# Optimization experiments

Measured on AMD Instinct MI355X. Metric: run time of the kernel, lower is better.

## Reference

```python
import jax, jax.numpy as jnp
import numpy as np

NUM_HEADS = 8


def setup_inputs() -> dict:
    key = jax.random.key(0)
    ks = jax.random.split(key, 7)
    B, D, N = 16, 512, 2048
    sc = 1.0 / np.sqrt(D)
    return {
        "X_Query": jax.random.normal(ks[0], (B, D, N), jnp.float32),
        "X_Key": jax.random.normal(ks[1], (B, D, N), jnp.float32),
        "X_Value": jax.random.normal(ks[2], (B, D, N), jnp.float32),
        "W_q": jax.random.normal(ks[3], (D, D), jnp.float32) * sc,
        "W_k": jax.random.normal(ks[4], (D, D), jnp.float32) * sc,
        "W_v": jax.random.normal(ks[5], (D, D), jnp.float32) * sc,
        "W_o": jax.random.normal(ks[6], (D, D), jnp.float32) * sc,
    }


def _proj(W, x):
    # Conv1d(D, D, kernel_size=1, bias=False) == channel matmul
    return jnp.einsum('oi,bin->bon', W, x)


def _split_heads(x, h):
    # torch: cat(x.chunk(h, dim=-1), dim=0) -> (h, B, D, N/h) stacked layout
    B, D, N = x.shape
    return x.reshape(B, D, h, N // h).transpose(2, 0, 1, 3)


def _mha(XQ, XK, XV, Wq, Wk, Wv, Wo):
    B, D, N = XQ.shape
    h = NUM_HEADS
    Nh = N // h
    q = _split_heads(_proj(Wq, XQ), h)  # (h, B, D, Nh)
    k = _split_heads(_proj(Wk, XK), h)
    v = _split_heads(_proj(Wv, XV), h)
    # scores over the CHANNEL axis: (h, B, D, D), scaled by sqrt(d_k)=sqrt(Nh)
    scores = jnp.einsum('hbdn,hben->hbde', q, k) / jnp.sqrt(jnp.asarray(Nh, q.dtype))
    p = jax.nn.softmax(scores, axis=-1)
    out = jnp.einsum('hbde,hben->hbdn', p, v)  # (h, B, D, Nh)
    # torch: cat(chunks, dim=0) inverse -> cat along dim=-1
    attn_heads = out.transpose(1, 2, 0, 3).reshape(B, D, N)
    return _proj(Wo, XQ - attn_heads)


def reference(X_Query, X_Key, X_Value, W_q, W_k, W_v, W_o):
    return _mha(X_Query, X_Key, X_Value, W_q, W_k, W_v, W_o)
```

## Files before the change

kernel.cpp:

```cpp
#include <hip/hip_runtime.h>
#include <hip/hip_bf16.h>

#define DD  512
#define NN  2048
#define BB  16
#define NHD 256

typedef unsigned short u16;
typedef __attribute__((ext_vector_type(4))) float f32x4;
typedef __attribute__((ext_vector_type(8))) short s16x8;
typedef __attribute__((ext_vector_type(4))) u16   u16x4;

static __device__ __forceinline__ u16 f2bf(float f) {
  __hip_bfloat16 h = __float2bfloat16(f);
  return *reinterpret_cast<u16*>(&h);
}
static __device__ __forceinline__ float bf2f(u16 u) {
  union { unsigned int i; float f; } v; v.i = ((unsigned int)u) << 16; return v.f;
}
static __device__ __forceinline__ f32x4 mfma_bf16(s16x8 a, s16x8 b, f32x4 c) {
  return __builtin_amdgcn_mfma_f32_16x16x32_bf16(a, b, c, 0, 0, 0);
}
static __device__ __forceinline__ void gload_lds16(const u16* g, u16* l) {
  __builtin_amdgcn_global_load_lds(
      (const __attribute__((address_space(1))) unsigned int*)g,
      (__attribute__((address_space(3))) unsigned int*)l, 16, 0, 0);
}
static __device__ __forceinline__ void barrier_raw() {
  __builtin_amdgcn_sched_barrier(0);
  __builtin_amdgcn_s_barrier();
  __builtin_amdgcn_sched_barrier(0);
}
#define WAITCNT(s) do { asm volatile("s_waitcnt " s ::: "memory"); \
                        __builtin_amdgcn_sched_barrier(0); } while (0)

__global__ __launch_bounds__(256) void k_cvt_w(const float* __restrict__ w0,
                                               const float* __restrict__ w1,
                                               const float* __restrict__ w2,
                                               const float* __restrict__ w3,
                                               u16* __restrict__ out) {
  const float* srcs[4] = {w0, w1, w2, w3};
  const float* s = srcs[blockIdx.y];
  u16* o = out + (size_t)blockIdx.y * (DD * DD);
  int idx = blockIdx.x * 256 + threadIdx.x;
  float4 v = *(const float4*)(s + (size_t)idx * 4);
  u16x4 u = {f2bf(v.x), f2bf(v.y), f2bf(v.z), f2bf(v.w)};
  *(u16x4*)(o + (size_t)idx * 4) = u;
}

__global__ __launch_bounds__(256) void k_transpose(const float* __restrict__ X,
                                                   u16* __restrict__ XT) {
  __shared__ float t[64][68];
  const int tid = threadIdx.x;
  const int n0 = blockIdx.x * 64, d0 = blockIdx.y * 64, b = blockIdx.z;
  const float* Xb = X + ((size_t)b * DD + d0) * NN + n0;
#pragma unroll
  for (int i = 0; i < 4; ++i) {
    int r = (tid >> 4) + i * 16;
    int c = (tid & 15) * 4;
    float4 v = *(const float4*)(Xb + (size_t)r * NN + c);
    t[r][c] = v.x; t[r][c + 1] = v.y; t[r][c + 2] = v.z; t[r][c + 3] = v.w;
  }
  __syncthreads();
  u16* Ob = XT + ((size_t)b * NN + n0) * DD + d0;
#pragma unroll
  for (int i = 0; i < 4; ++i) {
    int n = (tid >> 4) + i * 16;
    int d = (tid & 15) * 4;
    u16x4 u = {f2bf(t[d][n]), f2bf(t[d + 1][n]), f2bf(t[d + 2][n]), f2bf(t[d + 3][n])};
    *(u16x4*)(Ob + (size_t)n * DD + d) = u;
  }
}

#define GEMM_STAGE(Ag, lda, Bg, ldb, buf, kt)                                   \
  {                                                                             \
    _Pragma("unroll")                                                           \
    for (int j = 0; j < 4; ++j) {                                               \
      int s = j * 256 + w * 64 + lane;                                          \
      int row = s >> 3, u = s & 7;                                              \
      int col = ((u ^ (row & 7)) * 8);                                          \
      gload_lds16(Ag + (size_t)row * lda + (kt) * 64 + col, &Ab[buf][s * 8]);   \
      gload_lds16(Bg + (size_t)row * ldb + (kt) * 64 + col, &Bb[buf][s * 8]);   \
    }                                                                           \
  }

#define GEMM_COMPUTE(buf)                                                       \
  {                                                                             \
    _Pragma("unroll")                                                           \
    for (int ks = 0; ks < 2; ++ks) {                                            \
      s16x8 av[4], bv[4];                                                       \
      _Pragma("unroll")                                                         \
      for (int m = 0; m < 4; ++m) {                                             \
        int row = wm + m * 16 + r;                                              \
        av[m] = *(const s16x8*)&Ab[buf][row * 64 + (((ks * 4 + g) ^ (row & 7)) * 8)]; \
      }                                                                         \
      _Pragma("unroll")                                                         \
      for (int nf = 0; nf < 4; ++nf) {                                          \
        int row = wn + nf * 16 + r;                                             \
        bv[nf] = *(const s16x8*)&Bb[buf][row * 64 + (((ks * 4 + g) ^ (row & 7)) * 8)]; \
      }                                                                         \
      _Pragma("unroll")                                                         \
      for (int m = 0; m < 4; ++m)                                               \
        _Pragma("unroll")                                                       \
        for (int nf = 0; nf < 4; ++nf)                                          \
          acc[m][nf] = mfma_bf16(av[m], bv[nf], acc[m][nf]);                    \
    }                                                                           \
  }

#define GEMM_PREAMBLE                                                           \
  __shared__ __align__(16) u16 Ab[2][128 * 64];                                 \
  __shared__ __align__(16) u16 Bb[2][128 * 64];                                 \
  const int tid = threadIdx.x;                                                  \
  const int lane = tid & 63, w = tid >> 6;                                      \
  const int wm = (w >> 1) * 64, wn = (w & 1) * 64;                              \
  const int r = lane & 15, g = lane >> 4;                                       \
  f32x4 acc[4][4] = {};

#define GEMM_MAINLOOP(Ag, lda, Bg, ldb, nkt)                                    \
  GEMM_STAGE(Ag, lda, Bg, ldb, 0, 0);                                           \
  __syncthreads();                                                              \
  for (int kt = 0; kt < (nkt) - 1; ++kt) {                                      \
    GEMM_STAGE(Ag, lda, Bg, ldb, (kt & 1) ^ 1, kt + 1);                         \
    GEMM_COMPUTE(kt & 1);                                                       \
    __syncthreads();                                                            \
  }                                                                             \
  GEMM_COMPUTE(((nkt) - 1) & 1);

template <typename OUT_T>
__global__ __launch_bounds__(256) void k_gemm_nt(
    const u16* __restrict__ A, long long a_bs, int lda,
    const u16* __restrict__ B, long long b_bs, int ldb,
    OUT_T* __restrict__ C, long long c_bs, int ldc, int K) {
  GEMM_PREAMBLE
  const int m0 = blockIdx.x * 128, n0 = blockIdx.y * 128;
  const u16* Ag = A + (size_t)blockIdx.z * a_bs + (size_t)m0 * lda;
  const u16* Bg = B + (size_t)blockIdx.z * b_bs + (size_t)n0 * ldb;
  const int nkt = K >> 6;
  GEMM_MAINLOOP(Ag, lda, Bg, ldb, nkt);

  OUT_T* Cg = C + (size_t)blockIdx.z * c_bs;
#pragma unroll
  for (int m = 0; m < 4; ++m)
#pragma unroll
    for (int nf = 0; nf < 4; ++nf)
#pragma unroll
      for (int j = 0; j < 4; ++j) {
        int row = m0 + wm + m * 16 + g * 4 + j;
        int col = n0 + wn + nf * 16 + r;
        float v = acc[m][nf][j];
        if constexpr (sizeof(OUT_T) == 2) Cg[(size_t)row * ldc + col] = f2bf(v);
        else                              Cg[(size_t)row * ldc + col] = v;
      }
}

__global__ __launch_bounds__(512, 4) void k_attn_fused(
    const u16* __restrict__ Qdn, const u16* __restrict__ Kdn,
    const u16* __restrict__ VT,  const u16* __restrict__ XqT,
    u16* __restrict__ And) {
  __shared__ __align__(16) u16 L[26624];
  u16* Kr = L;
  u16* Vr = L + 12288;
  char* Psb = (char*)(L + 24576);

  const int tid = threadIdx.x;
  const int lane = tid & 63, w = tid >> 6;
  const int r = lane & 15, g = lane >> 4;
  const int dq = w >> 1, eh = w & 1;
  const int nq = w >> 1, dh = w & 1;
  const int bid = blockIdx.x;
  const int dt = bid >> 7, hb = bid & 127;
  const int h = hb & 7, b = hb >> 3;
  const int d0 = dt * 64, hn0 = h * NHD;

  const u16* Qg = Qdn + ((size_t)b * DD + d0) * NN + hn0;
  const u16* Kg = Kdn + ((size_t)b * DD) * NN + hn0;
  const u16* Vg = VT + ((size_t)b * NN + hn0) * DD;

  auto stage_k = [&](int s) {
    const int e0 = (s >> 1) * 32, n0 = (s & 1) * 128;
    u16* dst = Kr + (s % 3) * 4096;
    int row = tid >> 4, u = tid & 15;
    gload_lds16(Kg + (size_t)(e0 + row) * NN + n0 + ((u ^ (row & 7)) * 8), dst + tid * 8);
  };
  auto stage_v = [&](int t) {
    const int e0 = (t >> 1) * 32, j = t & 1;
    u16* dst = Vr + (t % 3) * 4096;
    int rl = tid >> 2, u = tid & 3;
    int gn = (rl >> 5) * 64 + j * 32 + (rl & 31);
    gload_lds16(Vg + (size_t)gn * DD + e0 + ((u ^ (rl & 3)) * 8), dst + tid * 8);
  };

#pragma unroll
  for (int jj = 0; jj < 4; ++jj) {
    int s = jj * 512 + tid;
    int row = s >> 5, u = s & 31;
    gload_lds16(Qg + (size_t)row * NN + ((u ^ (row & 7)) * 8), L + s * 8);
  }
  WAITCNT("vmcnt(0)");
  barrier_raw();
  s16x8 qf[8];
  {
    const int qrow = dq * 16 + r;
#pragma unroll
    for (int k2 = 0; k2 < 8; ++k2)
      qf[k2] = *(const s16x8*)&L[qrow * 256 + (((k2 * 4 + g) ^ (qrow & 7)) * 8)];
  }
  WAITCNT("lgkmcnt(0)");
  barrier_raw();
  stage_k(0); stage_v(0); stage_k(1);

  float psum[4] = {};
  f32x4 acc_o[2][2][2] = {};

  for (int et = 0; et < 16; ++et) {
    f32x4 acc_s = {};
#pragma unroll
    for (int cn = 0; cn < 2; ++cn) {
      const int s = et * 2 + cn;
      if (cn == 0)      WAITCNT("vmcnt(2)");
      else if (et < 15) WAITCNT("vmcnt(2)");
      else              WAITCNT("vmcnt(1)");
      barrier_raw();
      if (s + 1 < 32) stage_v(s + 1);
      if (s + 2 < 32) stage_k(s + 2);
      const u16* kb = Kr + (s % 3) * 4096;
      const int rowe = eh * 16 + r;
      __builtin_amdgcn_s_setprio(1);
#pragma unroll
      for (int kq = 0; kq < 4; ++kq) {
        s16x8 bv = *(const s16x8*)&kb[rowe * 128 + (((kq * 4 + g) ^ (rowe & 7)) * 8)];
        acc_s = mfma_bf16(qf[cn * 4 + kq], bv, acc_s);
      }
      __builtin_amdgcn_s_setprio(0);
      WAITCNT("lgkmcnt(0)");
    }
#pragma unroll
    for (int j = 0; j < 4; ++j) {
      int rowd = dq * 16 + g * 4 + j;
      int cole = eh * 16 + r;
      float p = __expf(acc_s[j] * 0.0625f);
      psum[j] += p;
      *(u16*)(Psb + rowd * 64 + (((cole * 2) ^ ((rowd & 3) << 4)))) = f2bf(p);
    }
    WAITCNT("lgkmcnt(0)");
    if (et < 15) WAITCNT("vmcnt(3)");
    else         WAITCNT("vmcnt(0)");
    barrier_raw();
#pragma unroll
    for (int j = 0; j < 2; ++j) {
      const u16* vb = Vr + ((et * 2 + j) % 3) * 4096;
      s16x8 pb[2];
#pragma unroll
      for (int nf = 0; nf < 2; ++nf) {
        int rowd = dh * 32 + nf * 16 + r;
        pb[nf] = *(const s16x8*)(Psb + rowd * 64 + ((g * 16) ^ ((rowd & 3) << 4)));
      }
      __builtin_amdgcn_s_setprio(1);
#pragma unroll
      for (int ms = 0; ms < 2; ++ms) {
        int rl = nq * 32 + ms * 16 + r;
        s16x8 av = *(const s16x8*)((const char*)vb + rl * 64 + ((g * 16) ^ ((rl & 3) << 4)));
        acc_o[j][ms][0] = mfma_bf16(av, pb[0], acc_o[j][ms][0]);
        acc_o[j][ms][1] = mfma_bf16(av, pb[1], acc_o[j][ms][1]);
      }
      __builtin_amdgcn_s_setprio(0);
    }
    WAITCNT("lgkmcnt(0)");
    barrier_raw();
  }

  float* rs = (float*)L;
#pragma unroll
  for (int j = 0; j < 4; ++j) {
    float v = psum[j];
    v += __shfl_xor(v, 1);
    v += __shfl_xor(v, 2);
    v += __shfl_xor(v, 4);
    v += __shfl_xor(v, 8);
    if (r == 0) rs[w * 16 + g * 4 + j] = v;
  }
  __syncthreads();
  if (tid < 64) {
    int dqi = tid >> 4, i = tid & 15;
    rs[128 + tid] = 1.0f / (rs[(dqi * 2) * 16 + i] + rs[(dqi * 2 + 1) * 16 + i]);
  }
  __syncthreads();

  const u16* Xg = XqT + ((size_t)b * NN + hn0) * DD + d0;
  u16* Ag = And + ((size_t)b * NN + hn0) * DD + d0;
#pragma unroll
  for (int j = 0; j < 2; ++j)
#pragma unroll
    for (int ms = 0; ms < 2; ++ms)
#pragma unroll
      for (int nf = 0; nf < 2; ++nf) {
        const int dc = dh * 32 + nf * 16 + r;
        const float inv = rs[128 + dc];
#pragma unroll
        for (int jj = 0; jj < 4; ++jj) {
          const int npos = nq * 64 + j * 32 + ms * 16 + g * 4 + jj;
          float o = acc_o[j][ms][nf][jj] * inv;
          float xq = bf2f(Xg[(size_t)npos * DD + dc]);
          Ag[(size_t)npos * DD + dc] = f2bf(xq - o);
        }
      }
}

extern "C" void kernel_launch(void* const* d_in, const int* in_sizes, int n_in,
                              void* d_out, int out_size, void* d_ws, size_t ws_size,
                              hipStream_t stream) {
  const float* Xq = (const float*)d_in[0];
  const float* Xk = (const float*)d_in[1];
  const float* Xv = (const float*)d_in[2];
  const float* Wq = (const float*)d_in[3];
  const float* Wk = (const float*)d_in[4];
  const float* Wv = (const float*)d_in[5];
  const float* Wo = (const float*)d_in[6];
  float* out = (float*)d_out;

  char* ws = (char*)d_ws;
  const size_t MB = 1024 * 1024;
  u16* Wb  = (u16*)ws;
  u16* XqT = (u16*)(ws + 2 * MB);
  u16* Z2  = (u16*)(ws + 34 * MB);
  u16* And = Z2;
  u16* Qdn = (u16*)(ws + 66 * MB);
  u16* VTb = (u16*)d_out;
  u16* Kdn = (u16*)d_out + (size_t)BB * NN * DD;

  k_cvt_w<<<dim3(256, 4), 256, 0, stream>>>(Wq, Wk, Wv, Wo, Wb);

  k_transpose<<<dim3(NN / 64, DD / 64, BB), 256, 0, stream>>>(Xv, Z2);
  k_gemm_nt<u16><<<dim3(NN / 128, DD / 128, BB), 256, 0, stream>>>(
      Z2, (long long)NN * DD, DD,
      Wb + 2 * DD * DD, 0, DD,
      VTb, (long long)NN * DD, DD, DD);

  k_transpose<<<dim3(NN / 64, DD / 64, BB), 256, 0, stream>>>(Xq, XqT);
  k_gemm_nt<u16><<<dim3(DD / 128, NN / 128, BB), 256, 0, stream>>>(
      Wb, 0, DD,
      XqT, (long long)NN * DD, DD,
      Qdn, (long long)DD * NN, NN, DD);

  k_transpose<<<dim3(NN / 64, DD / 64, BB), 256, 0, stream>>>(Xk, Z2);
  k_gemm_nt<u16><<<dim3(DD / 128, NN / 128, BB), 256, 0, stream>>>(
      Wb + 1 * DD * DD, 0, DD,
      Z2, (long long)NN * DD, DD,
      Kdn, (long long)DD * NN, NN, DD);

  k_attn_fused<<<dim3(1024), 512, 0, stream>>>(Qdn, Kdn, VTb, XqT, And);

  k_gemm_nt<float><<<dim3(DD / 128, NN / 128, BB), 256, 0, stream>>>(
      Wb + 3 * DD * DD, 0, DD,
      And, (long long)NN * DD, DD,
      out, (long long)DD * NN, NN, DD);
}
```

Baseline: 251.2 us.

## Merge three transposes into one launch and pad P tile instead of swizzling

The three separate fp32-to-bf16 transpose launches for Xq, Xk and Xv become one kernel launch with a 3x z-grid, which needs a separate workspace buffer for XkT. Independently, the P tile in shared memory inside the attention kernel switches from an XOR-swizzled 64-byte row layout to a padded row stride of 36 elements, read as two 8-byte loads. The first cuts launch overhead and tail effects. The second changes the LDS bank-conflict pattern and the number of load instructions, and may be neutral or worse for the P reads.

```diff
diff --git a/kernel.cpp b/kernel.cpp
--- a/kernel.cpp
+++ b/kernel.cpp
@@ -9,6 +9,7 @@
 typedef unsigned short u16;
 typedef __attribute__((ext_vector_type(4))) float f32x4;
 typedef __attribute__((ext_vector_type(8))) short s16x8;
+typedef __attribute__((ext_vector_type(4))) short s16x4;
 typedef __attribute__((ext_vector_type(4))) u16   u16x4;
 
 static __device__ __forceinline__ u16 f2bf(float f) {
@@ -48,11 +49,18 @@
   *(u16x4*)(o + (size_t)idx * 4) = u;
 }
 
-__global__ __launch_bounds__(256) void k_transpose(const float* __restrict__ X,
-                                                   u16* __restrict__ XT) {
+__global__ __launch_bounds__(256) void k_transpose3(const float* __restrict__ x0,
+                                                    const float* __restrict__ x1,
+                                                    const float* __restrict__ x2,
+                                                    u16* __restrict__ o0,
+                                                    u16* __restrict__ o1,
+                                                    u16* __restrict__ o2) {
   __shared__ float t[64][68];
   const int tid = threadIdx.x;
-  const int n0 = blockIdx.x * 64, d0 = blockIdx.y * 64, b = blockIdx.z;
+  const int z = blockIdx.z, which = z >> 4, b = z & 15;
+  const float* X = which == 0 ? x0 : (which == 1 ? x1 : x2);
+  u16*       XT = which == 0 ? o0 : (which == 1 ? o1 : o2);
+  const int n0 = blockIdx.x * 64, d0 = blockIdx.y * 64;
   const float* Xb = X + ((size_t)b * DD + d0) * NN + n0;
 #pragma unroll
   for (int i = 0; i < 4; ++i) {
@@ -157,10 +165,10 @@
     const u16* __restrict__ Qdn, const u16* __restrict__ Kdn,
     const u16* __restrict__ VT,  const u16* __restrict__ XqT,
     u16* __restrict__ And) {
-  __shared__ __align__(16) u16 L[26624];
+  __shared__ __align__(16) u16 L[26880];
   u16* Kr = L;
   u16* Vr = L + 12288;
-  char* Psb = (char*)(L + 24576);
+  u16* Ps = L + 24576;
 
   const int tid = threadIdx.x;
   const int lane = tid & 63, w = tid >> 6;
@@ -240,7 +248,7 @@
       int cole = eh * 16 + r;
       float p = __expf(acc_s[j] * 0.0625f);
       psum[j] += p;
-      *(u16*)(Psb + rowd * 64 + (((cole * 2) ^ ((rowd & 3) << 4)))) = f2bf(p);
+      Ps[rowd * 36 + cole] = f2bf(p);
     }
     WAITCNT("lgkmcnt(0)");
     if (et < 15) WAITCNT("vmcnt(3)");
@@ -253,7 +261,9 @@
 #pragma unroll
       for (int nf = 0; nf < 2; ++nf) {
         int rowd = dh * 32 + nf * 16 + r;
-        pb[nf] = *(const s16x8*)(Psb + rowd * 64 + ((g * 16) ^ ((rowd & 3) << 4)));
+        s16x4 plo = *(const s16x4*)&Ps[rowd * 36 + g * 8];
+        s16x4 phi = *(const s16x4*)&Ps[rowd * 36 + g * 8 + 4];
+        pb[nf] = __builtin_shufflevector(plo, phi, 0, 1, 2, 3, 4, 5, 6, 7);
       }
       __builtin_amdgcn_s_setprio(1);
 #pragma unroll
@@ -322,30 +332,29 @@
   const size_t MB = 1024 * 1024;
   u16* Wb  = (u16*)ws;
   u16* XqT = (u16*)(ws + 2 * MB);
-  u16* Z2  = (u16*)(ws + 34 * MB);
-  u16* And = Z2;
+  u16* XvT = (u16*)(ws + 34 * MB);
+  u16* And = XvT;
   u16* Qdn = (u16*)(ws + 66 * MB);
+  u16* XkT = (u16*)(ws + 98 * MB);
   u16* VTb = (u16*)d_out;
   u16* Kdn = (u16*)d_out + (size_t)BB * NN * DD;
 
   k_cvt_w<<<dim3(256, 4), 256, 0, stream>>>(Wq, Wk, Wv, Wo, Wb);
 
-  k_transpose<<<dim3(NN / 64, DD / 64, BB), 256, 0, stream>>>(Xv, Z2);
+  k_transpose3<<<dim3(NN / 64, DD / 64, BB * 3), 256, 0, stream>>>(
+      Xq, Xk, Xv, XqT, XkT, XvT);
+
   k_gemm_nt<u16><<<dim3(NN / 128, DD / 128, BB), 256, 0, stream>>>(
-      Z2, (long long)NN * DD, DD,
+      XvT, (long long)NN * DD, DD,
       Wb + 2 * DD * DD, 0, DD,
       VTb, (long long)NN * DD, DD, DD);
-
-  k_transpose<<<dim3(NN / 64, DD / 64, BB), 256, 0, stream>>>(Xq, XqT);
   k_gemm_nt<u16><<<dim3(DD / 128, NN / 128, BB), 256, 0, stream>>>(
       Wb, 0, DD,
       XqT, (long long)NN * DD, DD,
       Qdn, (long long)DD * NN, NN, DD);
-
-  k_transpose<<<dim3(NN / 64, DD / 64, BB), 256, 0, stream>>>(Xk, Z2);
   k_gemm_nt<u16><<<dim3(DD / 128, NN / 128, BB), 256, 0, stream>>>(
       Wb + 1 * DD * DD, 0, DD,
-      Z2, (long long)NN * DD, DD,
+      XkT, (long long)NN * DD, DD,
       Kdn, (long long)DD * NN, NN, DD);
 
   k_attn_fused<<<dim3(1024), 512, 0, stream>>>(Qdn, Kdn, VTb, XqT, And);
```

After: 247.4 us. Within noise of the previous version (-1.5%).
